# Performance work log

Hardware: AMD Instinct MI355X
Metric: run time of the kernel (lower is better)

Reference implementation:

```python
import jax, jax.numpy as jnp
import numpy as np

D = 512
P = 1024
E = 256
OUT = 500


def setup_inputs() -> dict:
    key = jax.random.key(0)
    ks = jax.random.split(key, 10)
    s = 1.0 / np.sqrt(D)
    s2 = 1.0 / np.sqrt(2 * D)
    return {
        "post": jax.random.normal(ks[0], (P, D), dtype=jnp.float32),
        "emoji": jax.random.normal(ks[1], (E, D), dtype=jnp.float32),
        "k1_w": jax.random.normal(ks[2], (D, D), dtype=jnp.float32) * s,
        "k1_b": jax.random.normal(ks[3], (D,), dtype=jnp.float32) * s,
        "k2_w": jax.random.normal(ks[4], (D, D), dtype=jnp.float32) * s,
        "k2_b": jax.random.normal(ks[5], (D,), dtype=jnp.float32) * s,
        "l1_w": jax.random.normal(ks[6], (2 * D, D), dtype=jnp.float32) * s2,
        "l1_b": jax.random.normal(ks[7], (D,), dtype=jnp.float32) * s2,
        "l2_w": jax.random.normal(ks[8], (D, OUT), dtype=jnp.float32) * s,
        "l2_b": jax.random.normal(ks[9], (D if False else OUT,), dtype=jnp.float32) * s,
    }


def reference(post, emoji, k1_w, k1_b, k2_w, k2_b, l1_w, l1_b, l2_w, l2_b):
    # k1/k2 projections: [P, D], [E, D]
    p = post @ k1_w + k1_b
    e = emoji @ k2_w + k2_b
    # l1 on concat([tile(p), tile(e)], -1) == p @ W1_post + e @ W1_emoji + b,
    # broadcast-added over the pairwise grid (same math, avoids explicit tile+cat)
    d = post.shape[1]
    pp = p @ l1_w[:d]   # [P, D]
    ee = e @ l1_w[d:]   # [E, D]
    h = jax.nn.relu(pp[:, None, :] + ee[None, :, :] + l1_b)  # [P, E, D]
    out = jax.nn.relu(h @ l2_w + l2_b)  # [P, E, OUT]
    return out
```

## Files before the change

### kernel.cpp

```cpp
#include <hip/hip_runtime.h>
#include <hip/hip_bf16.h>

#define D_DIM 512
#define P_DIM 1024
#define E_DIM 256
#define OUT_DIM 500

typedef __attribute__((ext_vector_type(8))) __bf16 bf16x8;
typedef __attribute__((ext_vector_type(4))) float f32x4;

__device__ __forceinline__ unsigned short f2bf(float f) {
    unsigned u = __builtin_bit_cast(unsigned, f);
    u += 0x7FFFu + ((u >> 16) & 1u);
    return (unsigned short)(u >> 16);
}

__device__ __forceinline__ unsigned pack2(float a, float b) {
    return (unsigned)f2bf(a) | ((unsigned)f2bf(b) << 16);
}

__global__ void cast_bf16_kernel(const float* __restrict__ in,
                                 unsigned short* __restrict__ out, int n) {
    int i = blockIdx.x * 256 + threadIdx.x;
    if (i < n) out[i] = f2bf(in[i]);
}

__global__ void transpose_cast_kernel(const float* __restrict__ in,
                                      unsigned short* __restrict__ out,
                                      int R, int C, int Cpad) {
    __shared__ float tile[32][33];
    int c0 = blockIdx.x * 32, r0 = blockIdx.y * 32;
    #pragma unroll
    for (int s = 0; s < 32; s += 8) {
        int r = r0 + threadIdx.y + s, c = c0 + threadIdx.x;
        tile[threadIdx.y + s][threadIdx.x] = (r < R && c < C) ? in[r * C + c] : 0.f;
    }
    __syncthreads();
    #pragma unroll
    for (int s = 0; s < 32; s += 8) {
        int c = c0 + threadIdx.y + s, r = r0 + threadIdx.x;
        if (c < Cpad && r < R) out[c * R + r] = f2bf(tile[threadIdx.x][threadIdx.y + s]);
    }
}

__device__ __forceinline__ void store_out(float* p, float v) { *p = v; }
__device__ __forceinline__ void store_out(unsigned short* p, float v) { *p = f2bf(v); }

template <typename OutT>
__global__ __launch_bounds__(256)
void gemm128_kernel(const unsigned short* __restrict__ A,
                    const unsigned short* __restrict__ Bt,
                    const float* __restrict__ bias,
                    OutT* __restrict__ Cd, int M, int N, int K) {
    __shared__ __align__(16) unsigned short As[128 * 40];
    __shared__ __align__(16) unsigned short Bs[128 * 40];
    const int t = threadIdx.x;
    const int m0 = blockIdx.x * 128, n0 = blockIdx.y * 128;
    const int r = t >> 1, kh = (t & 1) * 16;
    const int w = t >> 6, l = t & 63;
    const int wm = (w & 1) * 64, wn = (w >> 1) * 64;
    const int lr = l & 15, lq = l >> 4;

    f32x4 acc[4][4];
    #pragma unroll
    for (int a = 0; a < 4; a++)
        #pragma unroll
        for (int b = 0; b < 4; b++) acc[a][b] = (f32x4){0.f, 0.f, 0.f, 0.f};

    const unsigned short* aRow = &A[(m0 + r) * K];
    const unsigned short* bRow = &Bt[(n0 + r) * K];

    for (int k0 = 0; k0 < K; k0 += 32) {
        uint4 a0 = *reinterpret_cast<const uint4*>(&aRow[k0 + kh]);
        uint4 a1 = *reinterpret_cast<const uint4*>(&aRow[k0 + kh + 8]);
        uint4 b0 = *reinterpret_cast<const uint4*>(&bRow[k0 + kh]);
        uint4 b1 = *reinterpret_cast<const uint4*>(&bRow[k0 + kh + 8]);
        __syncthreads();
        *reinterpret_cast<uint4*>(&As[r * 40 + kh])     = a0;
        *reinterpret_cast<uint4*>(&As[r * 40 + kh + 8]) = a1;
        *reinterpret_cast<uint4*>(&Bs[r * 40 + kh])     = b0;
        *reinterpret_cast<uint4*>(&Bs[r * 40 + kh + 8]) = b1;
        __syncthreads();
        bf16x8 af[4], bfr[4];
        #pragma unroll
        for (int mi = 0; mi < 4; mi++)
            af[mi] = *reinterpret_cast<const bf16x8*>(&As[(wm + mi * 16 + lr) * 40 + lq * 8]);
        #pragma unroll
        for (int ni = 0; ni < 4; ni++)
            bfr[ni] = *reinterpret_cast<const bf16x8*>(&Bs[(wn + ni * 16 + lr) * 40 + lq * 8]);
        #pragma unroll
        for (int mi = 0; mi < 4; mi++)
            #pragma unroll
            for (int ni = 0; ni < 4; ni++)
                acc[mi][ni] = __builtin_amdgcn_mfma_f32_16x16x32_bf16(af[mi], bfr[ni], acc[mi][ni], 0, 0, 0);
    }

    #pragma unroll
    for (int ni = 0; ni < 4; ni++) {
        int n = n0 + wn + ni * 16 + lr;
        float bv = bias ? bias[n] : 0.f;
        #pragma unroll
        for (int mi = 0; mi < 4; mi++) {
            int m = m0 + wm + mi * 16 + lq * 4;
            #pragma unroll
            for (int rg = 0; rg < 4; rg++)
                store_out(&Cd[(m + rg) * N + n], acc[mi][ni][rg] + bv);
        }
    }
}

__global__ __launch_bounds__(256)
void pair_mlp_kernel(const float* __restrict__ pp, const float* __restrict__ ee,
                     const unsigned short* __restrict__ w2t,
                     const float* __restrict__ b2, float* __restrict__ out) {
    __shared__ __align__(16) unsigned short As[128 * 40];
    __shared__ __align__(16) unsigned short Bs[128 * 40];
    __shared__ float pps[D_DIM];

    const int t = threadIdx.x;
    const int mtile = blockIdx.x;
    const int n0 = blockIdx.y * 128;
    const int i = mtile >> 1;
    const int j0 = (mtile & 1) * 128;
    const long pairBase = (long)mtile * 128;

    const int r = t >> 1, kh = (t & 1) * 16;
    const int w = t >> 6, l = t & 63;
    const int wm = (w & 1) * 64, wn = (w >> 1) * 64;
    const int lr = l & 15, lq = l >> 4;

    pps[t] = pp[i * D_DIM + t];
    pps[t + 256] = pp[i * D_DIM + t + 256];

    f32x4 acc[4][4];
    #pragma unroll
    for (int a = 0; a < 4; a++)
        #pragma unroll
        for (int b = 0; b < 4; b++) acc[a][b] = (f32x4){0.f, 0.f, 0.f, 0.f};

    const float* eeRow = &ee[(j0 + r) * D_DIM];
    const unsigned short* wRow = &w2t[(n0 + r) * D_DIM];

    for (int k0 = 0; k0 < D_DIM; k0 += 32) {
        f32x4 ev0 = *reinterpret_cast<const f32x4*>(&eeRow[k0 + kh]);
        f32x4 ev1 = *reinterpret_cast<const f32x4*>(&eeRow[k0 + kh + 4]);
        f32x4 ev2 = *reinterpret_cast<const f32x4*>(&eeRow[k0 + kh + 8]);
        f32x4 ev3 = *reinterpret_cast<const f32x4*>(&eeRow[k0 + kh + 12]);
        uint4 wv0 = *reinterpret_cast<const uint4*>(&wRow[k0 + kh]);
        uint4 wv1 = *reinterpret_cast<const uint4*>(&wRow[k0 + kh + 8]);
        __syncthreads();
        f32x4 pv0 = *reinterpret_cast<const f32x4*>(&pps[k0 + kh]);
        f32x4 pv1 = *reinterpret_cast<const f32x4*>(&pps[k0 + kh + 4]);
        f32x4 pv2 = *reinterpret_cast<const f32x4*>(&pps[k0 + kh + 8]);
        f32x4 pv3 = *reinterpret_cast<const f32x4*>(&pps[k0 + kh + 12]);
        f32x4 s0 = pv0 + ev0, s1 = pv1 + ev1, s2 = pv2 + ev2, s3 = pv3 + ev3;
        #pragma unroll
        for (int x = 0; x < 4; x++) {
            s0[x] = s0[x] > 0.f ? s0[x] : 0.f;
            s1[x] = s1[x] > 0.f ? s1[x] : 0.f;
            s2[x] = s2[x] > 0.f ? s2[x] : 0.f;
            s3[x] = s3[x] > 0.f ? s3[x] : 0.f;
        }
        uint4 h0, h1;
        h0.x = pack2(s0[0], s0[1]); h0.y = pack2(s0[2], s0[3]);
        h0.z = pack2(s1[0], s1[1]); h0.w = pack2(s1[2], s1[3]);
        h1.x = pack2(s2[0], s2[1]); h1.y = pack2(s2[2], s2[3]);
        h1.z = pack2(s3[0], s3[1]); h1.w = pack2(s3[2], s3[3]);
        *reinterpret_cast<uint4*>(&As[r * 40 + kh])     = h0;
        *reinterpret_cast<uint4*>(&As[r * 40 + kh + 8]) = h1;
        *reinterpret_cast<uint4*>(&Bs[r * 40 + kh])     = wv0;
        *reinterpret_cast<uint4*>(&Bs[r * 40 + kh + 8]) = wv1;
        __syncthreads();
        bf16x8 af[4], bfr[4];
        #pragma unroll
        for (int mi = 0; mi < 4; mi++)
            af[mi] = *reinterpret_cast<const bf16x8*>(&As[(wm + mi * 16 + lr) * 40 + lq * 8]);
        #pragma unroll
        for (int ni = 0; ni < 4; ni++)
            bfr[ni] = *reinterpret_cast<const bf16x8*>(&Bs[(wn + ni * 16 + lr) * 40 + lq * 8]);
        #pragma unroll
        for (int mi = 0; mi < 4; mi++)
            #pragma unroll
            for (int ni = 0; ni < 4; ni++)
                acc[mi][ni] = __builtin_amdgcn_mfma_f32_16x16x32_bf16(af[mi], bfr[ni], acc[mi][ni], 0, 0, 0);
    }

    #pragma unroll
    for (int ni = 0; ni < 4; ni++) {
        int n = n0 + wn + ni * 16 + lr;
        bool valid = n < OUT_DIM;
        float bv = valid ? b2[n] : 0.f;
        #pragma unroll
        for (int mi = 0; mi < 4; mi++) {
            int row = wm + mi * 16 + lq * 4;
            float* op = &out[(pairBase + row) * OUT_DIM + n];
            if (valid) {
                #pragma unroll
                for (int rg = 0; rg < 4; rg++) {
                    float v = acc[mi][ni][rg] + bv;
                    op[(long)rg * OUT_DIM] = v > 0.f ? v : 0.f;
                }
            }
        }
    }
}

extern "C" void kernel_launch(void* const* d_in, const int* in_sizes, int n_in,
                              void* d_out, int out_size, void* d_ws, size_t ws_size,
                              hipStream_t stream) {
    const float* post  = (const float*)d_in[0];
    const float* emoji = (const float*)d_in[1];
    const float* k1_w  = (const float*)d_in[2];
    const float* k1_b  = (const float*)d_in[3];
    const float* k2_w  = (const float*)d_in[4];
    const float* k2_b  = (const float*)d_in[5];
    const float* l1_w  = (const float*)d_in[6];
    const float* l1_b  = (const float*)d_in[7];
    const float* l2_w  = (const float*)d_in[8];
    const float* l2_b  = (const float*)d_in[9];
    float* out = (float*)d_out;

    char* wp = (char*)d_ws;
    auto alloc = [&](size_t bytes) { char* q = wp; wp += (bytes + 255) & ~(size_t)255; return q; };
    unsigned short* post_bf  = (unsigned short*)alloc(P_DIM * D_DIM * 2);
    unsigned short* emoji_bf = (unsigned short*)alloc(E_DIM * D_DIM * 2);
    unsigned short* k1_wt    = (unsigned short*)alloc(D_DIM * D_DIM * 2);
    unsigned short* k2_wt    = (unsigned short*)alloc(D_DIM * D_DIM * 2);
    unsigned short* l1at     = (unsigned short*)alloc(D_DIM * D_DIM * 2);
    unsigned short* l1bt     = (unsigned short*)alloc(D_DIM * D_DIM * 2);
    unsigned short* w2t      = (unsigned short*)alloc(512 * 512 * 2);
    unsigned short* p_bf     = (unsigned short*)alloc(P_DIM * D_DIM * 2);
    unsigned short* e_bf     = (unsigned short*)alloc(E_DIM * D_DIM * 2);
    float* pp  = (float*)alloc(P_DIM * D_DIM * 4);
    float* eeb = (float*)alloc(E_DIM * D_DIM * 4);

    cast_bf16_kernel<<<P_DIM * D_DIM / 256, 256, 0, stream>>>(post, post_bf, P_DIM * D_DIM);
    cast_bf16_kernel<<<E_DIM * D_DIM / 256, 256, 0, stream>>>(emoji, emoji_bf, E_DIM * D_DIM);

    dim3 tb(32, 8);
    transpose_cast_kernel<<<dim3(16, 16), tb, 0, stream>>>(k1_w, k1_wt, 512, 512, 512);
    transpose_cast_kernel<<<dim3(16, 16), tb, 0, stream>>>(k2_w, k2_wt, 512, 512, 512);
    transpose_cast_kernel<<<dim3(16, 16), tb, 0, stream>>>(l1_w, l1at, 512, 512, 512);
    transpose_cast_kernel<<<dim3(16, 16), tb, 0, stream>>>(l1_w + 512 * 512, l1bt, 512, 512, 512);
    transpose_cast_kernel<<<dim3(16, 16), tb, 0, stream>>>(l2_w, w2t, 512, 500, 512);

    gemm128_kernel<unsigned short><<<dim3(8, 4), 256, 0, stream>>>(post_bf, k1_wt, k1_b, p_bf, 1024, 512, 512);
    gemm128_kernel<unsigned short><<<dim3(2, 4), 256, 0, stream>>>(emoji_bf, k2_wt, k2_b, e_bf, 256, 512, 512);
    gemm128_kernel<float><<<dim3(8, 4), 256, 0, stream>>>(p_bf, l1at, (const float*)nullptr, pp, 1024, 512, 512);
    gemm128_kernel<float><<<dim3(2, 4), 256, 0, stream>>>(e_bf, l1bt, l1_b, eeb, 256, 512, 512);

    pair_mlp_kernel<<<dim3(2048, 4), 256, 0, stream>>>(pp, eeb, w2t, l2_b, out);
}
```

Baseline: 886.7 us.

## Build full hidden tile once in LDS and sweep all output columns per block

The pair MLP kernel now builds the whole 128x512 relu(pp+ee) hidden tile in LDS once per block, converting with the packed bf16 instruction. It then loops over both 256-wide output halves with 512 threads, double-buffering W2 chunks through registers. Before, the hidden tile was recomputed for each of four N-blocks. This removes the 4x redundant ee loads and elementwise work, and the grid shrinks to 2048 blocks. In exchange the block uses about 150KB of LDS, which limits occupancy to one block per CU, and it adds extra barriers per iteration.

```diff
diff --git a/kernel.cpp b/kernel.cpp
--- a/kernel.cpp
+++ b/kernel.cpp
@@ -109,72 +109,73 @@
     }
 }
 
-__global__ __launch_bounds__(256)
+__global__ __launch_bounds__(512)
 void pair_mlp_kernel(const float* __restrict__ pp, const float* __restrict__ ee,
                      const unsigned short* __restrict__ w2t,
                      const float* __restrict__ b2, float* __restrict__ out) {
-    __shared__ __align__(16) unsigned short As[128 * 40];
-    __shared__ __align__(16) unsigned short Bs[128 * 40];
-    __shared__ float pps[D_DIM];
+    __shared__ __align__(16) unsigned short Hs[128 * 520];
+    __shared__ __align__(16) unsigned short Bs[256 * 40];
 
     const int t = threadIdx.x;
     const int mtile = blockIdx.x;
-    const int n0 = blockIdx.y * 128;
     const int i = mtile >> 1;
     const int j0 = (mtile & 1) * 128;
     const long pairBase = (long)mtile * 128;
+
+    {
+        const int rq = t >> 7;
+        const int c4 = (t & 127) * 4;
+        const f32x4 pv = *reinterpret_cast<const f32x4*>(&pp[i * D_DIM + c4]);
+        #pragma unroll 8
+        for (int it = 0; it < 32; ++it) {
+            int r = it * 4 + rq;
+            f32x4 ev = *reinterpret_cast<const f32x4*>(&ee[(j0 + r) * D_DIM + c4]);
+            f32x4 s = pv + ev;
+            #pragma unroll
+            for (int x = 0; x < 4; x++) s[x] = s[x] > 0.f ? s[x] : 0.f;
+            unsigned u0, u1;
+            asm("v_cvt_pk_bf16_f32 %0, %1, %2" : "=v"(u0) : "v"(s[0]), "v"(s[1]));
+            asm("v_cvt_pk_bf16_f32 %0, %1, %2" : "=v"(u1) : "v"(s[2]), "v"(s[3]));
+            uint2 hv; hv.x = u0; hv.y = u1;
+            *reinterpret_cast<uint2*>(&Hs[r * 520 + c4]) = hv;
+        }
+    }
 
     const int r = t >> 1, kh = (t & 1) * 16;
     const int w = t >> 6, l = t & 63;
     const int wm = (w & 1) * 64, wn = (w >> 1) * 64;
     const int lr = l & 15, lq = l >> 4;
 
-    pps[t] = pp[i * D_DIM + t];
-    pps[t + 256] = pp[i * D_DIM + t + 256];
-
     f32x4 acc[4][4];
     #pragma unroll
     for (int a = 0; a < 4; a++)
         #pragma unroll
         for (int b = 0; b < 4; b++) acc[a][b] = (f32x4){0.f, 0.f, 0.f, 0.f};
 
-    const float* eeRow = &ee[(j0 + r) * D_DIM];
-    const unsigned short* wRow = &w2t[(n0 + r) * D_DIM];
-
-    for (int k0 = 0; k0 < D_DIM; k0 += 32) {
-        f32x4 ev0 = *reinterpret_cast<const f32x4*>(&eeRow[k0 + kh]);
-        f32x4 ev1 = *reinterpret_cast<const f32x4*>(&eeRow[k0 + kh + 4]);
-        f32x4 ev2 = *reinterpret_cast<const f32x4*>(&eeRow[k0 + kh + 8]);
-        f32x4 ev3 = *reinterpret_cast<const f32x4*>(&eeRow[k0 + kh + 12]);
-        uint4 wv0 = *reinterpret_cast<const uint4*>(&wRow[k0 + kh]);
-        uint4 wv1 = *reinterpret_cast<const uint4*>(&wRow[k0 + kh + 8]);
-        __syncthreads();
-        f32x4 pv0 = *reinterpret_cast<const f32x4*>(&pps[k0 + kh]);
-        f32x4 pv1 = *reinterpret_cast<const f32x4*>(&pps[k0 + kh + 4]);
-        f32x4 pv2 = *reinterpret_cast<const f32x4*>(&pps[k0 + kh + 8]);
-        f32x4 pv3 = *reinterpret_cast<const f32x4*>(&pps[k0 + kh + 12]);
-        f32x4 s0 = pv0 + ev0, s1 = pv1 + ev1, s2 = pv2 + ev2, s3 = pv3 + ev3;
-        #pragma unroll
-        for (int x = 0; x < 4; x++) {
-            s0[x] = s0[x] > 0.f ? s0[x] : 0.f;
-            s1[x] = s1[x] > 0.f ? s1[x] : 0.f;
-            s2[x] = s2[x] > 0.f ? s2[x] : 0.f;
-            s3[x] = s3[x] > 0.f ? s3[x] : 0.f;
-        }
-        uint4 h0, h1;
-        h0.x = pack2(s0[0], s0[1]); h0.y = pack2(s0[2], s0[3]);
-        h0.z = pack2(s1[0], s1[1]); h0.w = pack2(s1[2], s1[3]);
-        h1.x = pack2(s2[0], s2[1]); h1.y = pack2(s2[2], s2[3]);
-        h1.z = pack2(s3[0], s3[1]); h1.w = pack2(s3[2], s3[3]);
-        *reinterpret_cast<uint4*>(&As[r * 40 + kh])     = h0;
-        *reinterpret_cast<uint4*>(&As[r * 40 + kh + 8]) = h1;
-        *reinterpret_cast<uint4*>(&Bs[r * 40 + kh])     = wv0;
-        *reinterpret_cast<uint4*>(&Bs[r * 40 + kh + 8]) = wv1;
-        __syncthreads();
+    const unsigned short* wRow = &w2t[r * D_DIM + kh];
+
+    uint4 c0 = *reinterpret_cast<const uint4*>(wRow);
+    uint4 c1 = *reinterpret_cast<const uint4*>(wRow + 8);
+    __syncthreads();
+    *reinterpret_cast<uint4*>(&Bs[r * 40 + kh])     = c0;
+    *reinterpret_cast<uint4*>(&Bs[r * 40 + kh + 8]) = c1;
+    __syncthreads();
+
+    for (int u = 0; u < 32; ++u) {
+        const int k0 = (u & 15) * 32;
+
+        uint4 n0v, n1v;
+        if (u < 31) {
+            const int un = u + 1;
+            const unsigned short* p = wRow + ((un >> 4) * 256) * D_DIM + (un & 15) * 32;
+            n0v = *reinterpret_cast<const uint4*>(p);
+            n1v = *reinterpret_cast<const uint4*>(p + 8);
+        }
+
         bf16x8 af[4], bfr[4];
         #pragma unroll
         for (int mi = 0; mi < 4; mi++)
-            af[mi] = *reinterpret_cast<const bf16x8*>(&As[(wm + mi * 16 + lr) * 40 + lq * 8]);
+            af[mi] = *reinterpret_cast<const bf16x8*>(&Hs[(wm + mi * 16 + lr) * 520 + k0 + lq * 8]);
         #pragma unroll
         for (int ni = 0; ni < 4; ni++)
             bfr[ni] = *reinterpret_cast<const bf16x8*>(&Bs[(wn + ni * 16 + lr) * 40 + lq * 8]);
@@ -183,25 +184,36 @@
             #pragma unroll
             for (int ni = 0; ni < 4; ni++)
                 acc[mi][ni] = __builtin_amdgcn_mfma_f32_16x16x32_bf16(af[mi], bfr[ni], acc[mi][ni], 0, 0, 0);
-    }
-
-    #pragma unroll
-    for (int ni = 0; ni < 4; ni++) {
-        int n = n0 + wn + ni * 16 + lr;
-        bool valid = n < OUT_DIM;
-        float bv = valid ? b2[n] : 0.f;
-        #pragma unroll
-        for (int mi = 0; mi < 4; mi++) {
-            int row = wm + mi * 16 + lq * 4;
-            float* op = &out[(pairBase + row) * OUT_DIM + n];
-            if (valid) {
+
+        __syncthreads();
+        if (u < 31) {
+            *reinterpret_cast<uint4*>(&Bs[r * 40 + kh])     = n0v;
+            *reinterpret_cast<uint4*>(&Bs[r * 40 + kh + 8]) = n1v;
+        }
+
+        if ((u & 15) == 15) {
+            const int nbase = (u >> 4) * 256;
+            #pragma unroll
+            for (int ni = 0; ni < 4; ni++) {
+                int n = nbase + wn + ni * 16 + lr;
+                if (n < OUT_DIM) {
+                    float bv = b2[n];
+                    #pragma unroll
+                    for (int mi = 0; mi < 4; mi++) {
+                        long m = pairBase + wm + mi * 16 + lq * 4;
+                        float* op = &out[m * OUT_DIM + n];
+                        #pragma unroll
+                        for (int rg = 0; rg < 4; rg++) {
+                            float v = acc[mi][ni][rg] + bv;
+                            op[(long)rg * OUT_DIM] = v > 0.f ? v : 0.f;
+                        }
+                    }
+                }
                 #pragma unroll
-                for (int rg = 0; rg < 4; rg++) {
-                    float v = acc[mi][ni][rg] + bv;
-                    op[(long)rg * OUT_DIM] = v > 0.f ? v : 0.f;
-                }
+                for (int mi = 0; mi < 4; mi++) acc[mi][ni] = (f32x4){0.f, 0.f, 0.f, 0.f};
             }
         }
+        __syncthreads();
     }
 }
 
@@ -249,5 +261,5 @@
     gemm128_kernel<float><<<dim3(8, 4), 256, 0, stream>>>(p_bf, l1at, (const float*)nullptr, pp, 1024, 512, 512);
     gemm128_kernel<float><<<dim3(2, 4), 256, 0, stream>>>(e_bf, l1bt, l1_b, eeb, 256, 512, 512);
 
-    pair_mlp_kernel<<<dim3(2048, 4), 256, 0, stream>>>(pp, eeb, w2t, l2_b, out);
-}
+    pair_mlp_kernel<<<dim3(2048), 512, 0, stream>>>(pp, eeb, w2t, l2_b, out);
+}
```

Result: slower. 946.6 us (+6.8%).

## Double-buffer LDS tiles in pair_mlp and use hardware bf16 pack conversion

Applied to the files above, without the earlier changes.

Restructures the pair MLP K-loop into a software pipeline with two LDS buffers. Global loads for step k+2 and the h-generation and LDS write for step k+1 are issued after the MFMAs of step k, which drops one barrier per iteration. The manual round-to-nearest bf16 packing is replaced with the v_cvt_pk_bf16_f32 instruction, cutting VALU work. In exchange, LDS use doubles and register pressure rises because prefetched values stay live across the MFMAs.

```diff
diff --git a/kernel.cpp b/kernel.cpp
--- a/kernel.cpp
+++ b/kernel.cpp
@@ -13,10 +13,6 @@
     unsigned u = __builtin_bit_cast(unsigned, f);
     u += 0x7FFFu + ((u >> 16) & 1u);
     return (unsigned short)(u >> 16);
-}
-
-__device__ __forceinline__ unsigned pack2(float a, float b) {
-    return (unsigned)f2bf(a) | ((unsigned)f2bf(b) << 16);
 }
 
 __global__ void cast_bf16_kernel(const float* __restrict__ in,
@@ -113,8 +109,8 @@
 void pair_mlp_kernel(const float* __restrict__ pp, const float* __restrict__ ee,
                      const unsigned short* __restrict__ w2t,
                      const float* __restrict__ b2, float* __restrict__ out) {
-    __shared__ __align__(16) unsigned short As[128 * 40];
-    __shared__ __align__(16) unsigned short Bs[128 * 40];
+    __shared__ __align__(16) unsigned short As[2][128 * 40];
+    __shared__ __align__(16) unsigned short Bs[2][128 * 40];
     __shared__ float pps[D_DIM];
 
     const int t = threadIdx.x;
@@ -141,49 +137,75 @@
     const float* eeRow = &ee[(j0 + r) * D_DIM];
     const unsigned short* wRow = &w2t[(n0 + r) * D_DIM];
 
-    for (int k0 = 0; k0 < D_DIM; k0 += 32) {
-        f32x4 ev0 = *reinterpret_cast<const f32x4*>(&eeRow[k0 + kh]);
-        f32x4 ev1 = *reinterpret_cast<const f32x4*>(&eeRow[k0 + kh + 4]);
-        f32x4 ev2 = *reinterpret_cast<const f32x4*>(&eeRow[k0 + kh + 8]);
-        f32x4 ev3 = *reinterpret_cast<const f32x4*>(&eeRow[k0 + kh + 12]);
-        uint4 wv0 = *reinterpret_cast<const uint4*>(&wRow[k0 + kh]);
-        uint4 wv1 = *reinterpret_cast<const uint4*>(&wRow[k0 + kh + 8]);
-        __syncthreads();
-        f32x4 pv0 = *reinterpret_cast<const f32x4*>(&pps[k0 + kh]);
-        f32x4 pv1 = *reinterpret_cast<const f32x4*>(&pps[k0 + kh + 4]);
-        f32x4 pv2 = *reinterpret_cast<const f32x4*>(&pps[k0 + kh + 8]);
-        f32x4 pv3 = *reinterpret_cast<const f32x4*>(&pps[k0 + kh + 12]);
-        f32x4 s0 = pv0 + ev0, s1 = pv1 + ev1, s2 = pv2 + ev2, s3 = pv3 + ev3;
-        #pragma unroll
-        for (int x = 0; x < 4; x++) {
-            s0[x] = s0[x] > 0.f ? s0[x] : 0.f;
-            s1[x] = s1[x] > 0.f ? s1[x] : 0.f;
-            s2[x] = s2[x] > 0.f ? s2[x] : 0.f;
-            s3[x] = s3[x] > 0.f ? s3[x] : 0.f;
-        }
-        uint4 h0, h1;
-        h0.x = pack2(s0[0], s0[1]); h0.y = pack2(s0[2], s0[3]);
-        h0.z = pack2(s1[0], s1[1]); h0.w = pack2(s1[2], s1[3]);
-        h1.x = pack2(s2[0], s2[1]); h1.y = pack2(s2[2], s2[3]);
-        h1.z = pack2(s3[0], s3[1]); h1.w = pack2(s3[2], s3[3]);
-        *reinterpret_cast<uint4*>(&As[r * 40 + kh])     = h0;
-        *reinterpret_cast<uint4*>(&As[r * 40 + kh + 8]) = h1;
-        *reinterpret_cast<uint4*>(&Bs[r * 40 + kh])     = wv0;
-        *reinterpret_cast<uint4*>(&Bs[r * 40 + kh + 8]) = wv1;
-        __syncthreads();
+    f32x4 ev0, ev1, ev2, ev3;
+    uint4 wv0, wv1;
+
+#define LOADK(K0) do {                                                        \
+        ev0 = *reinterpret_cast<const f32x4*>(&eeRow[(K0) + kh]);             \
+        ev1 = *reinterpret_cast<const f32x4*>(&eeRow[(K0) + kh + 4]);         \
+        ev2 = *reinterpret_cast<const f32x4*>(&eeRow[(K0) + kh + 8]);         \
+        ev3 = *reinterpret_cast<const f32x4*>(&eeRow[(K0) + kh + 12]);        \
+        wv0 = *reinterpret_cast<const uint4*>(&wRow[(K0) + kh]);              \
+        wv1 = *reinterpret_cast<const uint4*>(&wRow[(K0) + kh + 8]);          \
+    } while (0)
+
+#define HGEN_WRITE(BUF, K0) do {                                              \
+        f32x4 pv0 = *reinterpret_cast<const f32x4*>(&pps[(K0) + kh]);         \
+        f32x4 pv1 = *reinterpret_cast<const f32x4*>(&pps[(K0) + kh + 4]);     \
+        f32x4 pv2 = *reinterpret_cast<const f32x4*>(&pps[(K0) + kh + 8]);     \
+        f32x4 pv3 = *reinterpret_cast<const f32x4*>(&pps[(K0) + kh + 12]);    \
+        f32x4 s0 = pv0 + ev0, s1 = pv1 + ev1, s2 = pv2 + ev2, s3 = pv3 + ev3; \
+        _Pragma("unroll")                                                     \
+        for (int x = 0; x < 4; x++) {                                         \
+            s0[x] = s0[x] > 0.f ? s0[x] : 0.f;                                \
+            s1[x] = s1[x] > 0.f ? s1[x] : 0.f;                                \
+            s2[x] = s2[x] > 0.f ? s2[x] : 0.f;                                \
+            s3[x] = s3[x] > 0.f ? s3[x] : 0.f;                                \
+        }                                                                     \
+        uint4 h0, h1;                                                         \
+        asm("v_cvt_pk_bf16_f32 %0, %1, %2" : "=v"(h0.x) : "v"(s0[0]), "v"(s0[1])); \
+        asm("v_cvt_pk_bf16_f32 %0, %1, %2" : "=v"(h0.y) : "v"(s0[2]), "v"(s0[3])); \
+        asm("v_cvt_pk_bf16_f32 %0, %1, %2" : "=v"(h0.z) : "v"(s1[0]), "v"(s1[1])); \
+        asm("v_cvt_pk_bf16_f32 %0, %1, %2" : "=v"(h0.w) : "v"(s1[2]), "v"(s1[3])); \
+        asm("v_cvt_pk_bf16_f32 %0, %1, %2" : "=v"(h1.x) : "v"(s2[0]), "v"(s2[1])); \
+        asm("v_cvt_pk_bf16_f32 %0, %1, %2" : "=v"(h1.y) : "v"(s2[2]), "v"(s2[3])); \
+        asm("v_cvt_pk_bf16_f32 %0, %1, %2" : "=v"(h1.z) : "v"(s3[0]), "v"(s3[1])); \
+        asm("v_cvt_pk_bf16_f32 %0, %1, %2" : "=v"(h1.w) : "v"(s3[2]), "v"(s3[3])); \
+        *reinterpret_cast<uint4*>(&As[BUF][r * 40 + kh])     = h0;            \
+        *reinterpret_cast<uint4*>(&As[BUF][r * 40 + kh + 8]) = h1;            \
+        *reinterpret_cast<uint4*>(&Bs[BUF][r * 40 + kh])     = wv0;           \
+        *reinterpret_cast<uint4*>(&Bs[BUF][r * 40 + kh + 8]) = wv1;           \
+    } while (0)
+
+    LOADK(0);
+    __syncthreads();
+    HGEN_WRITE(0, 0);
+    LOADK(32);
+    __syncthreads();
+
+    for (int s = 0; s < 16; ++s) {
+        const int cur = s & 1;
         bf16x8 af[4], bfr[4];
         #pragma unroll
         for (int mi = 0; mi < 4; mi++)
-            af[mi] = *reinterpret_cast<const bf16x8*>(&As[(wm + mi * 16 + lr) * 40 + lq * 8]);
+            af[mi] = *reinterpret_cast<const bf16x8*>(&As[cur][(wm + mi * 16 + lr) * 40 + lq * 8]);
         #pragma unroll
         for (int ni = 0; ni < 4; ni++)
-            bfr[ni] = *reinterpret_cast<const bf16x8*>(&Bs[(wn + ni * 16 + lr) * 40 + lq * 8]);
+            bfr[ni] = *reinterpret_cast<const bf16x8*>(&Bs[cur][(wn + ni * 16 + lr) * 40 + lq * 8]);
         #pragma unroll
         for (int mi = 0; mi < 4; mi++)
             #pragma unroll
             for (int ni = 0; ni < 4; ni++)
                 acc[mi][ni] = __builtin_amdgcn_mfma_f32_16x16x32_bf16(af[mi], bfr[ni], acc[mi][ni], 0, 0, 0);
-    }
+
+        if (s < 15) {
+            HGEN_WRITE(cur ^ 1, (s + 1) * 32);
+            if (s < 14) LOADK((s + 2) * 32);
+        }
+        __syncthreads();
+    }
+#undef LOADK
+#undef HGEN_WRITE
 
     #pragma unroll
     for (int ni = 0; ni < 4; ni++) {
```

New measurement: 864.9 us. 2.5% less time.
